# Optimization experiments

Hardware: AMD Instinct MI355X
Metric: run time of the kernel (lower is better)

## Reference

```python
import jax, jax.numpy as jnp
import numpy as np

B, N, C = 4, 8192, 128
NPOINT, NSAMPLE = 2048, 32
RADIUS = 0.1
EPS = 1e-5  # BatchNorm eps (eval mode with running stats)


def setup_inputs() -> dict:
    key = jax.random.key(0)
    k1, k2, k3 = jax.random.split(key, 3)
    return {
        "points_coor": jax.random.uniform(k1, (B, 3, N), dtype=jnp.float32),
        "points_fea": jax.random.normal(k2, (B, C, N), dtype=jnp.float32),
        "W": jax.random.normal(k3, (2 * C, C + 3), dtype=jnp.float32) * 0.05,
        "b": jnp.zeros((2 * C,), jnp.float32),
        "gamma": jnp.ones((2 * C,), jnp.float32),
        "beta": jnp.zeros((2 * C,), jnp.float32),
        "bn_mean": jnp.zeros((2 * C,), jnp.float32),
        "bn_var": jnp.ones((2 * C,), jnp.float32),
    }


def _fps_single(xyz):
    """Farthest point sampling for one cloud. xyz: (N,3) -> (NPOINT,) int32.
    Deterministic start at index 0 (torch version starts at a random index)."""
    n = xyz.shape[0]

    def body(carry, _):
        dist, farthest = carry
        centroid = xyz[farthest]                      # (3,)
        d = jnp.sum((xyz - centroid) ** 2, axis=-1)   # (N,)
        dist = jnp.minimum(dist, d)
        nxt = jnp.argmax(dist).astype(jnp.int32)
        return (dist, nxt), farthest

    init = (jnp.full((n,), 1e10, xyz.dtype), jnp.int32(0))
    (_, _), idx = jax.lax.scan(body, init, None, length=NPOINT)
    return idx


def _gather(points, idx):
    # points: (B,N,D), idx: (B,S,K) -> (B,S,K,D)
    return jax.vmap(lambda p, i: p[i])(points, idx)


def reference(points_coor, points_fea, W, b, gamma, beta, bn_mean, bn_var):
    coor = points_coor.transpose(0, 2, 1)  # (B,N,3)
    fea = points_fea.transpose(0, 2, 1)    # (B,N,C)

    # S: farthest point sampling
    fps_idx = jax.vmap(_fps_single)(coor)                              # (B,S)
    new_coor = jnp.take_along_axis(coor, fps_idx[:, :, None], axis=1)  # (B,S,3)

    # G: hybrid knn/ball query -- k nearest, out-of-radius replaced by nearest
    sq = (jnp.sum(new_coor ** 2, -1)[:, :, None]
          + jnp.sum(coor ** 2, -1)[:, None, :]
          - 2.0 * jnp.einsum('bsd,bnd->bsn', new_coor, coor))           # (B,S,N)
    neg_d, idx = jax.lax.top_k(-sq, NSAMPLE)                            # k smallest
    d = -neg_d
    group_idx = jnp.where(d > RADIUS ** 2, idx[:, :, 0:1], idx)         # (B,S,K)

    g_coor = (_gather(coor, group_idx) - new_coor[:, :, None, :]) / RADIUS  # (B,S,K,3)
    g_fea = _gather(fea, group_idx)                                         # (B,S,K,C)
    g = jnp.concatenate([g_fea, g_coor], axis=-1)                           # (B,S,K,C+3)

    # P: shared 1x1 conv + BN(eval) + ReLU, then max-pool over neighbors
    h = jnp.einsum('bskc,dc->bskd', g, W) + b
    h = gamma * (h - bn_mean) * jax.lax.rsqrt(bn_var + EPS) + beta
    h = jax.nn.relu(h)
    new_fea = jnp.max(h, axis=2)  # (B,S,2C)

    return new_coor.transpose(0, 2, 1), new_fea.transpose(0, 2, 1)
```

## Files before the change

kernel.cpp:

```cpp
#include <hip/hip_runtime.h>
#include <stdint.h>


typedef unsigned short u16;
typedef unsigned long long u64;
typedef __bf16 bf16x8 __attribute__((ext_vector_type(8)));
typedef float f32x4 __attribute__((ext_vector_type(4)));
typedef float f32x2 __attribute__((ext_vector_type(2)));

#define NB 4
#define NPTS 8192
#define CH 128
#define SPTS 2048
#define KN 32
#define CINP 160

__device__ __forceinline__ u16 f2b(float f) {
    unsigned x = __float_as_uint(f);
    unsigned r = (x + 0x7fffu + ((x >> 16) & 1u)) >> 16;
    return (u16)r;
}
__device__ __forceinline__ u64 umin64(u64 a, u64 b) { return a < b ? a : b; }
__device__ __forceinline__ int mort3(int v) {
    return (v & 1) | ((v & 2) << 2) | ((v & 4) << 4);
}

template <int CTRL>
__device__ __forceinline__ u64 dpp_max64(u64 k) {
    unsigned lo = (unsigned)k, hi = (unsigned)(k >> 32);
    unsigned mlo = (unsigned)__builtin_amdgcn_update_dpp((int)lo, (int)lo, CTRL, 0xF, 0xF, false);
    unsigned mhi = (unsigned)__builtin_amdgcn_update_dpp((int)hi, (int)hi, CTRL, 0xF, 0xF, false);
    u64 m = ((u64)mhi << 32) | mlo;
    return m > k ? m : k;
}
template <int CTRL>
__device__ __forceinline__ unsigned dpp_maxu(unsigned v) {
    unsigned mv = (unsigned)__builtin_amdgcn_update_dpp((int)v, (int)v, CTRL, 0xF, 0xF, false);
    return mv > v ? mv : v;
}

__global__ __launch_bounds__(256) void ksort(const float* __restrict__ coor,
                                             float* __restrict__ sxg,
                                             float* __restrict__ syg,
                                             float* __restrict__ szg,
                                             int* __restrict__ sog) {
    __shared__ int hist[512], base[512];
    int b = blockIdx.x, tid = threadIdx.x;
    const float* cb = coor + b * 3 * NPTS;
    hist[tid] = 0;
    hist[tid + 256] = 0;
    __syncthreads();
    int bins[32];
#pragma unroll 4
    for (int i = 0; i < 32; ++i) {
        int n = tid * 32 + i;
        float x = cb[n], y = cb[NPTS + n], z = cb[2 * NPTS + n];
        int bx = min(7, (int)(x * 8.0f));
        int by = min(7, (int)(y * 8.0f));
        int bz = min(7, (int)(z * 8.0f));
        int bin = mort3(bx) | (mort3(by) << 1) | (mort3(bz) << 2);
        bins[i] = bin;
        atomicAdd(&hist[bin], 1);
    }
    __syncthreads();
    if (tid == 0) {
        int acc = 0;
        for (int k2 = 0; k2 < 512; ++k2) { base[k2] = acc; acc += hist[k2]; hist[k2] = 0; }
    }
    __syncthreads();
#pragma unroll 4
    for (int i = 0; i < 32; ++i) {
        int n = tid * 32 + i;
        int bin = bins[i];
        int pos = base[bin] + atomicAdd(&hist[bin], 1);
        sxg[b * NPTS + pos] = cb[n];
        syg[b * NPTS + pos] = cb[NPTS + n];
        szg[b * NPTS + pos] = cb[2 * NPTS + n];
        sog[b * NPTS + pos] = n;
    }
}

__global__ __launch_bounds__(1024) void kfps(const float* __restrict__ sxg,
                                             const float* __restrict__ syg,
                                             const float* __restrict__ szg,
                                             const int* __restrict__ sog,
                                             int* __restrict__ fpsIdx,
                                             float* __restrict__ outCoor,
                                             const float* __restrict__ fea,
                                             const float* __restrict__ coor,
                                             const float* __restrict__ W,
                                             u16* __restrict__ feaT,
                                             float* __restrict__ pp,
                                             u16* __restrict__ Wpad) {
    __shared__ float4 sp[NPTS];
    __shared__ unsigned sWin[SPTS];
    __shared__ u64 sAtom[4];
    __shared__ int slot0s;
    int bid = blockIdx.x;
    int tid = threadIdx.x;
    if (bid >= 4) {
        if (bid < 68) {
            u16(*T)[130] = (u16(*)[130])sp;
            int base_t = (bid - 4) * 4;
#pragma unroll 1
            for (int k = 0; k < 4; ++k) {
                int tidx = base_t + k;
                int b = tidx >> 6, nt = tidx & 63;
                int n0 = nt * 128;
#pragma unroll 4
                for (int it = 0; it < 16; ++it) {
                    int idx = it * 1024 + tid;
                    int c = idx >> 7, nl = idx & 127;
                    T[nl][c] = f2b(fea[((size_t)(b * CH + c)) * NPTS + n0 + nl]);
                }
                __syncthreads();
#pragma unroll 4
                for (int it = 0; it < 16; ++it) {
                    int idx = it * 1024 + tid;
                    int nl = idx >> 7, c = idx & 127;
                    feaT[((size_t)(b * NPTS + n0 + nl)) * CH + c] = T[nl][c];
                }
                __syncthreads();
            }
        } else if (bid < 100) {
            int gid = (bid - 68) * 1024 + tid;
            int n = gid & 8191, b = gid >> 13;
            const float* cb = coor + b * 3 * NPTS;
            float x = cb[n], y = cb[NPTS + n], z = cb[2 * NPTS + n];
            pp[gid] = __fadd_rn(__fadd_rn(__fmul_rn(x, x), __fmul_rn(y, y)),
                                __fmul_rn(z, z));
        } else {
            int i = (bid - 100) * 1024 + tid;
            int d = i / CINP, k = i - d * CINP;
            Wpad[i] = (k < 131) ? f2b(W[d * 131 + k]) : (u16)0;
        }
        return;
    }
    int b = bid;
    int lane = tid & 63;
    const float* gx = sxg + b * NPTS;
    const float* gy = syg + b * NPTS;
    const float* gz = szg + b * NPTS;
    const int* go = sog + b * NPTS;
    f32x2 X2[4], Y2[4], Z2[4], D2[4];
    unsigned PK[8];
    int n0 = tid * 8;
    if (tid < 4) sAtom[tid] = 0;
    float lox, hix, loy, hiy, loz, hiz;
#pragma unroll
    for (int j = 0; j < 8; ++j) {
        float x = gx[n0 + j], y = gy[n0 + j], z = gz[n0 + j];
        sp[n0 + j] = make_float4(x, y, z, 0.0f);
        X2[j >> 1][j & 1] = x; Y2[j >> 1][j & 1] = y; Z2[j >> 1][j & 1] = z;
        D2[j >> 1][j & 1] = 1e10f;
        int oi = go[n0 + j];
        PK[j] = ((unsigned)oi << 16) | (unsigned)(n0 + j);
        if (oi == 0) slot0s = n0 + j;
        if (j == 0) {
            lox = hix = x; loy = hiy = y; loz = hiz = z;
        } else {
            lox = fminf(lox, x); hix = fmaxf(hix, x);
            loy = fminf(loy, y); hiy = fmaxf(hiy, y);
            loz = fminf(loz, z); hiz = fmaxf(hiz, z);
        }
    }
    __syncthreads();
    int far = slot0s;
    if (tid == 0) sWin[0] = (unsigned)slot0s;
    float lm = 3.4e38f;
    u64 cachedKey = 1;
    for (int t = 1; t < SPTS; ++t) {
        float4 c = sp[far];
        float fx = c.x, fy = c.y, fz = c.z;
        float ddx = fmaxf(0.0f, fmaxf(lox - fx, fx - hix));
        float ddy = fmaxf(0.0f, fmaxf(loy - fy, fy - hiy));
        float ddz = fmaxf(0.0f, fmaxf(loz - fz, fz - hiz));
        float dmin2 = ddx * ddx + ddy * ddy + ddz * ddz;
        if (__ballot(dmin2 * 0.9995f < lm) != 0ull) {
            {
#pragma clang fp contract(off)
                f32x2 fx2 = {fx, fx}, fy2 = {fy, fy}, fz2 = {fz, fz};
#pragma unroll
                for (int i = 0; i < 4; ++i) {
                    f32x2 dx = X2[i] - fx2;
                    f32x2 dy = Y2[i] - fy2;
                    f32x2 dz = Z2[i] - fz2;
                    f32x2 s = (dx * dx + dy * dy) + dz * dz;
                    D2[i] = __builtin_elementwise_min(D2[i], s);
                }
            }
            f32x2 t01 = __builtin_elementwise_max(D2[0], D2[1]);
            f32x2 t23 = __builtin_elementwise_max(D2[2], D2[3]);
            f32x2 t03 = __builtin_elementwise_max(t01, t23);
            float m = fmaxf(t03[0], t03[1]);
            lm = m;
            unsigned sel = 0xFFFFFFFFu;
#pragma unroll
            for (int j = 0; j < 8; ++j) {
                float dj = D2[j >> 1][j & 1];
                sel = (dj == m) ? (sel < PK[j] ? sel : PK[j]) : sel;
            }
            unsigned mbits = __float_as_uint(m);
            unsigned r = mbits;
            r = dpp_maxu<0xB1>(r);
            r = dpp_maxu<0x4E>(r);
            r = dpp_maxu<0x141>(r);
            r = dpp_maxu<0x140>(r);
            r = dpp_maxu<0x142>(r);
            r = dpp_maxu<0x143>(r);
            unsigned wmaxb = (unsigned)__builtin_amdgcn_readlane((int)r, 63);
            u64 ball = __ballot(mbits == wmaxb);
            unsigned wpk;
            if (__popcll(ball) == 1) {
                int l = __ffsll(ball) - 1;
                wpk = (unsigned)__builtin_amdgcn_readlane((int)sel, l);
            } else {
                u64 kk = (mbits == wmaxb) ? (((u64)wmaxb << 32) | (unsigned)~sel) : 0ull;
                kk = dpp_max64<0xB1>(kk);
                kk = dpp_max64<0x4E>(kk);
                kk = dpp_max64<0x141>(kk);
                kk = dpp_max64<0x140>(kk);
                kk = dpp_max64<0x142>(kk);
                kk = dpp_max64<0x143>(kk);
                unsigned lo = (unsigned)__builtin_amdgcn_readlane((int)(unsigned)kk, 63);
                wpk = ~lo;
            }
            cachedKey = ((u64)wmaxb << 32) | (unsigned)~wpk;
        }
        if (lane == 63) atomicMax(&sAtom[t & 3], cachedKey);
        if (tid == 0) sAtom[(t + 1) & 3] = 0;
        __syncthreads();
        u64 wk = sAtom[t & 3];
        unsigned pk = ~(unsigned)wk;
        far = (int)(pk & 0xFFFFu);
        if (tid == 0) sWin[t] = pk;
    }
    __syncthreads();
    for (int i = tid; i < SPTS; i += 1024) {
        unsigned pk = sWin[i];
        int slot = (int)(pk & 0xFFFFu);
        float4 c = sp[slot];
        fpsIdx[b * SPTS + i] = (int)(pk >> 16);
        float* oc = outCoor + b * 3 * SPTS + i;
        oc[0] = c.x; oc[SPTS] = c.y; oc[2 * SPTS] = c.z;
    }
}

__global__ __launch_bounds__(256) void kgroup(const float* __restrict__ coor,
                                              const float* __restrict__ pp,
                                              const int* __restrict__ fpsIdx,
                                              int* __restrict__ gidxOut) {
    __shared__ u64 buf[4][256];
    __shared__ int cnt[4];
    int tid = threadIdx.x;
    int wv = tid >> 6, lane = tid & 63;
    if (tid < 4) cnt[tid] = 0;
    __syncthreads();
    int row = blockIdx.x * 4 + wv;
    int b = row >> 11, s = row & 2047;
    const float* cb = coor + b * 3 * NPTS;
    int n0 = fpsIdx[b * SPTS + s];
    float cx = cb[n0], cy = cb[NPTS + n0], cz = cb[2 * NPTS + n0];
    float cc = __fadd_rn(__fadd_rn(__fmul_rn(cx, cx), __fmul_rn(cy, cy)),
                         __fmul_rn(cz, cz));
    const float* ppb = pp + b * NPTS;
    u64 mk = ~0ull;
    for (int n = lane; n < NPTS; n += 64) {
        float x = cb[n], y = cb[NPTS + n], z = cb[2 * NPTS + n];
        float dot = __fmaf_rn(cz, z, __fmaf_rn(cy, y, __fmul_rn(cx, x)));
        float sq = __fsub_rn(__fadd_rn(cc, ppb[n]), __fmul_rn(2.0f, dot));
        unsigned ub = __float_as_uint(sq);
        ub ^= (ub >> 31) ? 0xFFFFFFFFu : 0x80000000u;
        u64 key = ((u64)ub << 32) | (unsigned)n;
        mk = umin64(mk, key);
        if (sq <= 0.01f) {
            int p = atomicAdd(&cnt[wv], 1);
            if (p < 256) buf[wv][p] = key;
        }
    }
#pragma unroll
    for (int off = 32; off > 0; off >>= 1) mk = umin64(mk, __shfl_xor(mk, off));
    int C = cnt[wv];
    if (C > 256) C = 256;
    int* go = gidxOut + row * KN;
    if (C <= 32) {
        if (lane < 32) {
            unsigned idx = (lane < C) ? (unsigned)buf[wv][lane] : (unsigned)mk;
            go[lane] = (int)idx;
        }
    } else {
        u64 e[4];
#pragma unroll
        for (int i = 0; i < 4; ++i) {
            int j2 = lane + (i << 6);
            e[i] = (j2 < C) ? buf[wv][j2] : ~0ull;
        }
        int cl = 0;
        unsigned sel = 0;
        for (int it = 0; it < 32; ++it) {
            u64 lb = ~0ull;
            int li = 0;
#pragma unroll
            for (int i = 0; i < 4; ++i) {
                bool f = (((cl >> i) & 1) == 0) && (e[i] < lb);
                lb = f ? e[i] : lb;
                li = f ? i : li;
            }
            u64 wmin = lb;
#pragma unroll
            for (int off = 32; off > 0; off >>= 1) wmin = umin64(wmin, __shfl_xor(wmin, off));
            u64 bal = __ballot(lb == wmin);
            int src = __ffsll((unsigned long long)bal) - 1;
            if (lane == src) cl |= (1 << li);
            if (lane == it) sel = (unsigned)wmin;
        }
        if (lane < 32) go[lane] = (int)sel;
    }
}

__global__ __launch_bounds__(256) void kfeat(const float* __restrict__ coor,
                                             const u16* __restrict__ feaT,
                                             const u16* __restrict__ Wpad,
                                             const float* __restrict__ bias,
                                             const float* __restrict__ gamma,
                                             const float* __restrict__ beta,
                                             const float* __restrict__ bmean,
                                             const float* __restrict__ bvar,
                                             const int* __restrict__ fpsIdx,
                                             const int* __restrict__ gidx,
                                             float* __restrict__ outFea) {
    __shared__ u16 g[KN][168];
    int row = blockIdx.x;
    int b = row >> 11, s = row & 2047;
    int tid = threadIdx.x;
    {
        int k = tid >> 3, j = tid & 7;
        const float* cb = coor + b * 3 * NPTS;
        int nc = fpsIdx[b * SPTS + s];
        int nbr = gidx[row * KN + k];
        const uint4* f4 = (const uint4*)(feaT + (((size_t)b * NPTS + nbr) << 7));
        uint4* gr = (uint4*)&g[k][0];
        gr[j] = f4[j];
        gr[j + 8] = f4[j + 8];
        for (int c = 128 + j; c < CINP; c += 8) {
            u16 v = 0;
            if (c < 131) {
                int dim = c - 128;
                float pv = cb[dim * NPTS + nbr];
                float cv = cb[dim * NPTS + nc];
                v = f2b(__fdiv_rn(__fsub_rn(pv, cv), 0.1f));
            }
            g[k][c] = v;
        }
    }
    __syncthreads();
    int w = tid >> 6, lane = tid & 63;
    int mrow = lane & 15, q = lane >> 4;
    f32x4 acc[4][2] = {};
#pragma unroll
    for (int ks = 0; ks < 5; ++ks) {
        int kb = ks * 32 + q * 8;
        bf16x8 b0 = *(const bf16x8*)&g[mrow][kb];
        bf16x8 b1 = *(const bf16x8*)&g[mrow + 16][kb];
#pragma unroll
        for (int mt = 0; mt < 4; ++mt) {
            bf16x8 a = *(const bf16x8*)&Wpad[(size_t)(w * 64 + mt * 16 + mrow) * CINP + kb];
            acc[mt][0] = __builtin_amdgcn_mfma_f32_16x16x32_bf16(a, b0, acc[mt][0], 0, 0, 0);
            acc[mt][1] = __builtin_amdgcn_mfma_f32_16x16x32_bf16(a, b1, acc[mt][1], 0, 0, 0);
        }
    }
#pragma unroll
    for (int mt = 0; mt < 4; ++mt) {
#pragma unroll
        for (int r = 0; r < 4; ++r) {
            int m = w * 64 + mt * 16 + q * 4 + r;
            float ga = gamma[m], be = beta[m];
            float mu = bmean[m], va = bvar[m], bi = bias[m];
            float rs = 1.0f / sqrtf(va + 1e-5f);
            float h0 = acc[mt][0][r] + bi;
            h0 = fmaxf(ga * (h0 - mu) * rs + be, 0.0f);
            float h1 = acc[mt][1][r] + bi;
            h1 = fmaxf(ga * (h1 - mu) * rs + be, 0.0f);
            float v = fmaxf(h0, h1);
#pragma unroll
            for (int off = 1; off < 16; off <<= 1) v = fmaxf(v, __shfl_xor(v, off));
            if (mrow == 0) outFea[((size_t)(b * 256 + m)) * SPTS + s] = v;
        }
    }
}

extern "C" void kernel_launch(void* const* d_in, const int* in_sizes, int n_in,
                              void* d_out, int out_size, void* d_ws, size_t ws_size,
                              hipStream_t stream) {
    const float* coor = (const float*)d_in[0];
    const float* fea = (const float*)d_in[1];
    const float* W = (const float*)d_in[2];
    const float* bias = (const float*)d_in[3];
    const float* gamma = (const float*)d_in[4];
    const float* beta = (const float*)d_in[5];
    const float* bmean = (const float*)d_in[6];
    const float* bvar = (const float*)d_in[7];
    char* ws = (char*)d_ws;
    int* fpsIdx = (int*)ws;
    int* gidx = (int*)(ws + 32768);
    float* pp = (float*)(ws + 32768 + 1048576);
    u16* feaT = (u16*)(ws + 1212416);
    u16* Wpad = (u16*)(ws + 9601024);
    float* sxg = (float*)(ws + 9682944);
    float* syg = (float*)(ws + 9814016);
    float* szg = (float*)(ws + 9945088);
    int* sog = (int*)(ws + 10076160);
    float* outC = (float*)d_out;
    float* outF = outC + NB * 3 * SPTS;

    ksort<<<NB, 256, 0, stream>>>(coor, sxg, syg, szg, sog);
    kfps<<<140, 1024, 0, stream>>>(sxg, syg, szg, sog, fpsIdx, outC,
                                   fea, coor, W, feaT, pp, Wpad);
    kgroup<<<2048, 256, 0, stream>>>(coor, pp, fpsIdx, gidx);
    kfeat<<<8192, 256, 0, stream>>>(coor, feaT, Wpad, bias, gamma, beta, bmean, bvar,
                                    fpsIdx, gidx, outF);
}
```

Measured before the change: 1.528 ms.

## Fuse FPS, grouping and feature MLP into one persistent kernel with progress counters

```diff
diff --git a/kernel.cpp b/kernel.cpp
--- a/kernel.cpp
+++ b/kernel.cpp
@@ -43,9 +43,11 @@
                                              float* __restrict__ sxg,
                                              float* __restrict__ syg,
                                              float* __restrict__ szg,
-                                             int* __restrict__ sog) {
+                                             int* __restrict__ sog,
+                                             int* __restrict__ ctrs) {
     __shared__ int hist[512], base[512];
     int b = blockIdx.x, tid = threadIdx.x;
+    if (b == 0 && tid < 8) ctrs[tid] = 0;
     const float* cb = coor + b * 3 * NPTS;
     hist[tid] = 0;
     hist[tid + 256] = 0;
@@ -80,59 +82,217 @@
     }
 }
 
-__global__ __launch_bounds__(1024) void kfps(const float* __restrict__ sxg,
-                                             const float* __restrict__ syg,
-                                             const float* __restrict__ szg,
-                                             const int* __restrict__ sog,
-                                             int* __restrict__ fpsIdx,
-                                             float* __restrict__ outCoor,
-                                             const float* __restrict__ fea,
-                                             const float* __restrict__ coor,
-                                             const float* __restrict__ W,
-                                             u16* __restrict__ feaT,
-                                             float* __restrict__ pp,
-                                             u16* __restrict__ Wpad) {
+__global__ __launch_bounds__(1024) void kmega(const float* __restrict__ sxg,
+                                              const float* __restrict__ syg,
+                                              const float* __restrict__ szg,
+                                              const int* __restrict__ sog,
+                                              int* __restrict__ fpsIdx,
+                                              float* __restrict__ outCoor,
+                                              const float* __restrict__ fea,
+                                              const float* __restrict__ coor,
+                                              const float* __restrict__ W,
+                                              u16* __restrict__ feaT,
+                                              float* __restrict__ pp,
+                                              u16* __restrict__ Wpad,
+                                              const float* __restrict__ bias,
+                                              const float* __restrict__ gamma,
+                                              const float* __restrict__ beta,
+                                              const float* __restrict__ bmean,
+                                              const float* __restrict__ bvar,
+                                              float* __restrict__ outFea,
+                                              int* __restrict__ ctrs) {
     __shared__ float4 sp[NPTS];
     __shared__ unsigned sWin[SPTS];
     __shared__ u64 sAtom[4];
     __shared__ int slot0s;
+    __shared__ int sBase;
     int bid = blockIdx.x;
     int tid = threadIdx.x;
+
     if (bid >= 4) {
-        if (bid < 68) {
-            u16(*T)[130] = (u16(*)[130])sp;
-            int base_t = (bid - 4) * 4;
-#pragma unroll 1
-            for (int k = 0; k < 4; ++k) {
-                int tidx = base_t + k;
-                int b = tidx >> 6, nt = tidx & 63;
+        int wid = bid - 4;
+        for (int c = wid; c < 328; c += 252) {
+            if (c < 256) {
+                u16(*T)[130] = (u16(*)[130])sp;
+                int b = c >> 6, nt = c & 63;
                 int n0 = nt * 128;
 #pragma unroll 4
                 for (int it = 0; it < 16; ++it) {
                     int idx = it * 1024 + tid;
-                    int c = idx >> 7, nl = idx & 127;
-                    T[nl][c] = f2b(fea[((size_t)(b * CH + c)) * NPTS + n0 + nl]);
+                    int cc = idx >> 7, nl = idx & 127;
+                    T[nl][cc] = f2b(fea[((size_t)(b * CH + cc)) * NPTS + n0 + nl]);
                 }
                 __syncthreads();
 #pragma unroll 4
                 for (int it = 0; it < 16; ++it) {
                     int idx = it * 1024 + tid;
-                    int nl = idx >> 7, c = idx & 127;
-                    feaT[((size_t)(b * NPTS + n0 + nl)) * CH + c] = T[nl][c];
-                }
+                    int nl = idx >> 7, cc = idx & 127;
+                    feaT[((size_t)(b * NPTS + n0 + nl)) * CH + cc] = T[nl][cc];
+                }
+            } else if (c < 288) {
+                int gid = (c - 256) * 1024 + tid;
+                int n = gid & 8191, b = gid >> 13;
+                const float* cb = coor + b * 3 * NPTS;
+                float x = cb[n], y = cb[NPTS + n], z = cb[2 * NPTS + n];
+                pp[gid] = __fadd_rn(__fadd_rn(__fmul_rn(x, x), __fmul_rn(y, y)),
+                                    __fmul_rn(z, z));
+            } else {
+                int i = (c - 288) * 1024 + tid;
+                int d = i / CINP, k = i - d * CINP;
+                Wpad[i] = (k < 131) ? f2b(W[d * 131 + k]) : (u16)0;
+            }
+            __syncthreads();
+        }
+        __threadfence();
+        __syncthreads();
+        if (tid == 0) {
+            atomicAdd(&ctrs[4], 1);
+            while (__hip_atomic_load(&ctrs[4], __ATOMIC_ACQUIRE,
+                                     __HIP_MEMORY_SCOPE_AGENT) < 252)
+                __builtin_amdgcn_s_sleep(8);
+        }
+        __syncthreads();
+        u64(*buf)[256] = (u64(*)[256])sp;
+        int* cnt = (int*)((char*)sp + 32768);
+        unsigned(*gsel)[KN] = (unsigned(*)[KN])((char*)sp + 32896);
+        u16(*g4)[KN][168] = (u16(*)[KN][168])((char*)sp + 34944);
+        int wv = tid >> 6, lane = tid & 63;
+        for (;;) {
+            if (tid == 0) sBase = atomicAdd(&ctrs[5], 16);
+            __syncthreads();
+            int lbase = sBase;
+            if (lbase >= NB * SPTS) break;
+            if (tid == 0) {
+                int need = ((lbase + 15) >> 2) + 1;
+                for (int bb = 0; bb < 4; ++bb)
+                    while (__hip_atomic_load(&ctrs[bb], __ATOMIC_ACQUIRE,
+                                             __HIP_MEMORY_SCOPE_AGENT) < need)
+                        __builtin_amdgcn_s_sleep(8);
+            }
+            __syncthreads();
+            {
+                int r = lbase + wv, bb = r & 3, s = r >> 2;
+                if (lane == 0) cnt[wv] = 0;
+                const float* cb = coor + bb * 3 * NPTS;
+                int n0 = fpsIdx[bb * SPTS + s];
+                float cx = cb[n0], cy = cb[NPTS + n0], cz = cb[2 * NPTS + n0];
+                float cc = __fadd_rn(__fadd_rn(__fmul_rn(cx, cx), __fmul_rn(cy, cy)),
+                                     __fmul_rn(cz, cz));
+                const float* ppb = pp + bb * NPTS;
+                u64 mk = ~0ull;
+                for (int n = lane; n < NPTS; n += 64) {
+                    float x = cb[n], y = cb[NPTS + n], z = cb[2 * NPTS + n];
+                    float dot = __fmaf_rn(cz, z, __fmaf_rn(cy, y, __fmul_rn(cx, x)));
+                    float sq = __fsub_rn(__fadd_rn(cc, ppb[n]), __fmul_rn(2.0f, dot));
+                    unsigned ub = __float_as_uint(sq);
+                    ub ^= (ub >> 31) ? 0xFFFFFFFFu : 0x80000000u;
+                    u64 key = ((u64)ub << 32) | (unsigned)n;
+                    mk = umin64(mk, key);
+                    if (sq <= 0.01f) {
+                        int p = atomicAdd(&cnt[wv], 1);
+                        if (p < 256) buf[wv][p] = key;
+                    }
+                }
+#pragma unroll
+                for (int off = 32; off > 0; off >>= 1) mk = umin64(mk, __shfl_xor(mk, off));
+                int C = cnt[wv];
+                if (C > 256) C = 256;
+                if (C <= 32) {
+                    if (lane < 32) {
+                        unsigned idx = (lane < C) ? (unsigned)buf[wv][lane] : (unsigned)mk;
+                        gsel[wv][lane] = idx;
+                    }
+                } else {
+                    u64 e[4];
+#pragma unroll
+                    for (int i = 0; i < 4; ++i) {
+                        int j2 = lane + (i << 6);
+                        e[i] = (j2 < C) ? buf[wv][j2] : ~0ull;
+                    }
+                    int cl = 0;
+                    unsigned sel = 0;
+                    for (int it = 0; it < 32; ++it) {
+                        u64 lb = ~0ull;
+                        int li = 0;
+#pragma unroll
+                        for (int i = 0; i < 4; ++i) {
+                            bool f = (((cl >> i) & 1) == 0) && (e[i] < lb);
+                            lb = f ? e[i] : lb;
+                            li = f ? i : li;
+                        }
+                        u64 wmin = lb;
+#pragma unroll
+                        for (int off = 32; off > 0; off >>= 1)
+                            wmin = umin64(wmin, __shfl_xor(wmin, off));
+                        u64 bal = __ballot(lb == wmin);
+                        int src = __ffsll((unsigned long long)bal) - 1;
+                        if (lane == src) cl |= (1 << li);
+                        if (lane == it) sel = (unsigned)wmin;
+                    }
+                    if (lane < 32) gsel[wv][lane] = sel;
+                }
+            }
+            __syncthreads();
+            for (int it4 = 0; it4 < 4; ++it4) {
                 __syncthreads();
-            }
-        } else if (bid < 100) {
-            int gid = (bid - 68) * 1024 + tid;
-            int n = gid & 8191, b = gid >> 13;
-            const float* cb = coor + b * 3 * NPTS;
-            float x = cb[n], y = cb[NPTS + n], z = cb[2 * NPTS + n];
-            pp[gid] = __fadd_rn(__fadd_rn(__fmul_rn(x, x), __fmul_rn(y, y)),
-                                __fmul_rn(z, z));
-        } else {
-            int i = (bid - 100) * 1024 + tid;
-            int d = i / CINP, k = i - d * CINP;
-            Wpad[i] = (k < 131) ? f2b(W[d * 131 + k]) : (u16)0;
+                int g256 = tid >> 8, t256 = tid & 255;
+                int rloc = it4 * 4 + g256;
+                int r2 = lbase + rloc, b2 = r2 & 3, s2 = r2 >> 2;
+                {
+                    int k = t256 >> 3, j = t256 & 7;
+                    const float* cb2 = coor + b2 * 3 * NPTS;
+                    int nc = fpsIdx[b2 * SPTS + s2];
+                    int nbr = (int)gsel[rloc][k];
+                    const uint4* f4p = (const uint4*)(feaT + (((size_t)b2 * NPTS + nbr) << 7));
+                    uint4* gr = (uint4*)&g4[g256][k][0];
+                    gr[j] = f4p[j];
+                    gr[j + 8] = f4p[j + 8];
+                    for (int cch = 128 + j; cch < CINP; cch += 8) {
+                        u16 v = 0;
+                        if (cch < 131) {
+                            int dim = cch - 128;
+                            float pv = cb2[dim * NPTS + nbr];
+                            float cv = cb2[dim * NPTS + nc];
+                            v = f2b(__fdiv_rn(__fsub_rn(pv, cv), 0.1f));
+                        }
+                        g4[g256][k][cch] = v;
+                    }
+                }
+                __syncthreads();
+                int w = t256 >> 6, lane2 = t256 & 63;
+                int mrow = lane2 & 15, q = lane2 >> 4;
+                f32x4 acc[4][2] = {};
+#pragma unroll
+                for (int ks = 0; ks < 5; ++ks) {
+                    int kb = ks * 32 + q * 8;
+                    bf16x8 b0 = *(const bf16x8*)&g4[g256][mrow][kb];
+                    bf16x8 b1 = *(const bf16x8*)&g4[g256][mrow + 16][kb];
+#pragma unroll
+                    for (int mt = 0; mt < 4; ++mt) {
+                        bf16x8 a = *(const bf16x8*)&Wpad[(size_t)(w * 64 + mt * 16 + mrow) * CINP + kb];
+                        acc[mt][0] = __builtin_amdgcn_mfma_f32_16x16x32_bf16(a, b0, acc[mt][0], 0, 0, 0);
+                        acc[mt][1] = __builtin_amdgcn_mfma_f32_16x16x32_bf16(a, b1, acc[mt][1], 0, 0, 0);
+                    }
+                }
+#pragma unroll
+                for (int mt = 0; mt < 4; ++mt) {
+#pragma unroll
+                    for (int r = 0; r < 4; ++r) {
+                        int m = w * 64 + mt * 16 + q * 4 + r;
+                        float ga = gamma[m], be = beta[m];
+                        float mu = bmean[m], va = bvar[m], bi = bias[m];
+                        float rs = 1.0f / sqrtf(va + 1e-5f);
+                        float h0 = acc[mt][0][r] + bi;
+                        h0 = fmaxf(ga * (h0 - mu) * rs + be, 0.0f);
+                        float h1 = acc[mt][1][r] + bi;
+                        h1 = fmaxf(ga * (h1 - mu) * rs + be, 0.0f);
+                        float v = fmaxf(h0, h1);
+#pragma unroll
+                        for (int off = 1; off < 16; off <<= 1) v = fmaxf(v, __shfl_xor(v, off));
+                        if (mrow == 0) outFea[((size_t)(b2 * 256 + m)) * SPTS + s2] = v;
+                    }
+                }
+            }
         }
         return;
     }
@@ -234,158 +394,31 @@
         unsigned pk = ~(unsigned)wk;
         far = (int)(pk & 0xFFFFu);
         if (tid == 0) sWin[t] = pk;
+        if ((t & 63) == 0 && tid < 64) {
+            int i = t - 64 + tid;
+            unsigned pk2 = sWin[i];
+            int slot = (int)(pk2 & 0xFFFFu);
+            float4 c4 = sp[slot];
+            fpsIdx[b * SPTS + i] = (int)(pk2 >> 16);
+            float* oc = outCoor + b * 3 * SPTS + i;
+            oc[0] = c4.x; oc[SPTS] = c4.y; oc[2 * SPTS] = c4.z;
+            __threadfence();
+            if (tid == 0)
+                __hip_atomic_store(&ctrs[b], t, __ATOMIC_RELEASE, __HIP_MEMORY_SCOPE_AGENT);
+        }
     }
     __syncthreads();
-    for (int i = tid; i < SPTS; i += 1024) {
-        unsigned pk = sWin[i];
-        int slot = (int)(pk & 0xFFFFu);
-        float4 c = sp[slot];
-        fpsIdx[b * SPTS + i] = (int)(pk >> 16);
+    if (tid < 64) {
+        int i = 1984 + tid;
+        unsigned pk2 = sWin[i];
+        int slot = (int)(pk2 & 0xFFFFu);
+        float4 c4 = sp[slot];
+        fpsIdx[b * SPTS + i] = (int)(pk2 >> 16);
         float* oc = outCoor + b * 3 * SPTS + i;
-        oc[0] = c.x; oc[SPTS] = c.y; oc[2 * SPTS] = c.z;
-    }
-}
-
-__global__ __launch_bounds__(256) void kgroup(const float* __restrict__ coor,
-                                              const float* __restrict__ pp,
-                                              const int* __restrict__ fpsIdx,
-                                              int* __restrict__ gidxOut) {
-    __shared__ u64 buf[4][256];
-    __shared__ int cnt[4];
-    int tid = threadIdx.x;
-    int wv = tid >> 6, lane = tid & 63;
-    if (tid < 4) cnt[tid] = 0;
-    __syncthreads();
-    int row = blockIdx.x * 4 + wv;
-    int b = row >> 11, s = row & 2047;
-    const float* cb = coor + b * 3 * NPTS;
-    int n0 = fpsIdx[b * SPTS + s];
-    float cx = cb[n0], cy = cb[NPTS + n0], cz = cb[2 * NPTS + n0];
-    float cc = __fadd_rn(__fadd_rn(__fmul_rn(cx, cx), __fmul_rn(cy, cy)),
-                         __fmul_rn(cz, cz));
-    const float* ppb = pp + b * NPTS;
-    u64 mk = ~0ull;
-    for (int n = lane; n < NPTS; n += 64) {
-        float x = cb[n], y = cb[NPTS + n], z = cb[2 * NPTS + n];
-        float dot = __fmaf_rn(cz, z, __fmaf_rn(cy, y, __fmul_rn(cx, x)));
-        float sq = __fsub_rn(__fadd_rn(cc, ppb[n]), __fmul_rn(2.0f, dot));
-        unsigned ub = __float_as_uint(sq);
-        ub ^= (ub >> 31) ? 0xFFFFFFFFu : 0x80000000u;
-        u64 key = ((u64)ub << 32) | (unsigned)n;
-        mk = umin64(mk, key);
-        if (sq <= 0.01f) {
-            int p = atomicAdd(&cnt[wv], 1);
-            if (p < 256) buf[wv][p] = key;
-        }
-    }
-#pragma unroll
-    for (int off = 32; off > 0; off >>= 1) mk = umin64(mk, __shfl_xor(mk, off));
-    int C = cnt[wv];
-    if (C > 256) C = 256;
-    int* go = gidxOut + row * KN;
-    if (C <= 32) {
-        if (lane < 32) {
-            unsigned idx = (lane < C) ? (unsigned)buf[wv][lane] : (unsigned)mk;
-            go[lane] = (int)idx;
-        }
-    } else {
-        u64 e[4];
-#pragma unroll
-        for (int i = 0; i < 4; ++i) {
-            int j2 = lane + (i << 6);
-            e[i] = (j2 < C) ? buf[wv][j2] : ~0ull;
-        }
-        int cl = 0;
-        unsigned sel = 0;
-        for (int it = 0; it < 32; ++it) {
-            u64 lb = ~0ull;
-            int li = 0;
-#pragma unroll
-            for (int i = 0; i < 4; ++i) {
-                bool f = (((cl >> i) & 1) == 0) && (e[i] < lb);
-                lb = f ? e[i] : lb;
-                li = f ? i : li;
-            }
-            u64 wmin = lb;
-#pragma unroll
-            for (int off = 32; off > 0; off >>= 1) wmin = umin64(wmin, __shfl_xor(wmin, off));
-            u64 bal = __ballot(lb == wmin);
-            int src = __ffsll((unsigned long long)bal) - 1;
-            if (lane == src) cl |= (1 << li);
-            if (lane == it) sel = (unsigned)wmin;
-        }
-        if (lane < 32) go[lane] = (int)sel;
-    }
-}
-
-__global__ __launch_bounds__(256) void kfeat(const float* __restrict__ coor,
-                                             const u16* __restrict__ feaT,
-                                             const u16* __restrict__ Wpad,
-                                             const float* __restrict__ bias,
-                                             const float* __restrict__ gamma,
-                                             const float* __restrict__ beta,
-                                             const float* __restrict__ bmean,
-                                             const float* __restrict__ bvar,
-                                             const int* __restrict__ fpsIdx,
-                                             const int* __restrict__ gidx,
-                                             float* __restrict__ outFea) {
-    __shared__ u16 g[KN][168];
-    int row = blockIdx.x;
-    int b = row >> 11, s = row & 2047;
-    int tid = threadIdx.x;
-    {
-        int k = tid >> 3, j = tid & 7;
-        const float* cb = coor + b * 3 * NPTS;
-        int nc = fpsIdx[b * SPTS + s];
-        int nbr = gidx[row * KN + k];
-        const uint4* f4 = (const uint4*)(feaT + (((size_t)b * NPTS + nbr) << 7));
-        uint4* gr = (uint4*)&g[k][0];
-        gr[j] = f4[j];
-        gr[j + 8] = f4[j + 8];
-        for (int c = 128 + j; c < CINP; c += 8) {
-            u16 v = 0;
-            if (c < 131) {
-                int dim = c - 128;
-                float pv = cb[dim * NPTS + nbr];
-                float cv = cb[dim * NPTS + nc];
-                v = f2b(__fdiv_rn(__fsub_rn(pv, cv), 0.1f));
-            }
-            g[k][c] = v;
-        }
-    }
-    __syncthreads();
-    int w = tid >> 6, lane = tid & 63;
-    int mrow = lane & 15, q = lane >> 4;
-    f32x4 acc[4][2] = {};
-#pragma unroll
-    for (int ks = 0; ks < 5; ++ks) {
-        int kb = ks * 32 + q * 8;
-        bf16x8 b0 = *(const bf16x8*)&g[mrow][kb];
-        bf16x8 b1 = *(const bf16x8*)&g[mrow + 16][kb];
-#pragma unroll
-        for (int mt = 0; mt < 4; ++mt) {
-            bf16x8 a = *(const bf16x8*)&Wpad[(size_t)(w * 64 + mt * 16 + mrow) * CINP + kb];
-            acc[mt][0] = __builtin_amdgcn_mfma_f32_16x16x32_bf16(a, b0, acc[mt][0], 0, 0, 0);
-            acc[mt][1] = __builtin_amdgcn_mfma_f32_16x16x32_bf16(a, b1, acc[mt][1], 0, 0, 0);
-        }
-    }
-#pragma unroll
-    for (int mt = 0; mt < 4; ++mt) {
-#pragma unroll
-        for (int r = 0; r < 4; ++r) {
-            int m = w * 64 + mt * 16 + q * 4 + r;
-            float ga = gamma[m], be = beta[m];
-            float mu = bmean[m], va = bvar[m], bi = bias[m];
-            float rs = 1.0f / sqrtf(va + 1e-5f);
-            float h0 = acc[mt][0][r] + bi;
-            h0 = fmaxf(ga * (h0 - mu) * rs + be, 0.0f);
-            float h1 = acc[mt][1][r] + bi;
-            h1 = fmaxf(ga * (h1 - mu) * rs + be, 0.0f);
-            float v = fmaxf(h0, h1);
-#pragma unroll
-            for (int off = 1; off < 16; off <<= 1) v = fmaxf(v, __shfl_xor(v, off));
-            if (mrow == 0) outFea[((size_t)(b * 256 + m)) * SPTS + s] = v;
-        }
+        oc[0] = c4.x; oc[SPTS] = c4.y; oc[2 * SPTS] = c4.z;
+        __threadfence();
+        if (tid == 0)
+            __hip_atomic_store(&ctrs[b], 2048, __ATOMIC_RELEASE, __HIP_MEMORY_SCOPE_AGENT);
     }
 }
 
@@ -402,21 +435,19 @@
     const float* bvar = (const float*)d_in[7];
     char* ws = (char*)d_ws;
     int* fpsIdx = (int*)ws;
-    int* gidx = (int*)(ws + 32768);
-    float* pp = (float*)(ws + 32768 + 1048576);
-    u16* feaT = (u16*)(ws + 1212416);
-    u16* Wpad = (u16*)(ws + 9601024);
-    float* sxg = (float*)(ws + 9682944);
-    float* syg = (float*)(ws + 9814016);
-    float* szg = (float*)(ws + 9945088);
-    int* sog = (int*)(ws + 10076160);
+    int* ctrs = (int*)(ws + 32768);
+    float* pp = (float*)(ws + 65536);
+    u16* feaT = (u16*)(ws + 1048576);
+    u16* Wpad = (u16*)(ws + 9437184);
+    float* sxg = (float*)(ws + 9519104);
+    float* syg = (float*)(ws + 9650176);
+    float* szg = (float*)(ws + 9781248);
+    int* sog = (int*)(ws + 9912320);
     float* outC = (float*)d_out;
     float* outF = outC + NB * 3 * SPTS;
 
-    ksort<<<NB, 256, 0, stream>>>(coor, sxg, syg, szg, sog);
-    kfps<<<140, 1024, 0, stream>>>(sxg, syg, szg, sog, fpsIdx, outC,
-                                   fea, coor, W, feaT, pp, Wpad);
-    kgroup<<<2048, 256, 0, stream>>>(coor, pp, fpsIdx, gidx);
-    kfeat<<<8192, 256, 0, stream>>>(coor, feaT, Wpad, bias, gamma, beta, bmean, bvar,
-                                    fpsIdx, gidx, outF);
-}
+    ksort<<<NB, 256, 0, stream>>>(coor, sxg, syg, szg, sog, ctrs);
+    kmega<<<256, 1024, 0, stream>>>(sxg, syg, szg, sog, fpsIdx, outC,
+                                    fea, coor, W, feaT, pp, Wpad,
+                                    bias, gamma, beta, bmean, bvar, outF, ctrs);
+}
```

New measurement: 1.727 ms. 13.0% more time.

## Use Morton-binned sorted points to prune kgroup neighbor search to nearby cells

Applied to the files above, without the earlier changes.

```diff
diff --git a/kernel.cpp b/kernel.cpp
--- a/kernel.cpp
+++ b/kernel.cpp
@@ -14,6 +14,7 @@
 #define SPTS 2048
 #define KN 32
 #define CINP 160
+#define GCAP 1280
 
 __device__ __forceinline__ u16 f2b(float f) {
     unsigned x = __float_as_uint(f);
@@ -43,7 +44,9 @@
                                              float* __restrict__ sxg,
                                              float* __restrict__ syg,
                                              float* __restrict__ szg,
-                                             int* __restrict__ sog) {
+                                             int* __restrict__ sog,
+                                             float* __restrict__ spp,
+                                             int* __restrict__ gbase) {
     __shared__ int hist[512], base[512];
     int b = blockIdx.x, tid = threadIdx.x;
     const float* cb = coor + b * 3 * NPTS;
@@ -68,15 +71,21 @@
         for (int k2 = 0; k2 < 512; ++k2) { base[k2] = acc; acc += hist[k2]; hist[k2] = 0; }
     }
     __syncthreads();
+    gbase[b * 513 + tid] = base[tid];
+    gbase[b * 513 + 256 + tid] = base[256 + tid];
+    if (tid == 0) gbase[b * 513 + 512] = NPTS;
 #pragma unroll 4
     for (int i = 0; i < 32; ++i) {
         int n = tid * 32 + i;
         int bin = bins[i];
         int pos = base[bin] + atomicAdd(&hist[bin], 1);
-        sxg[b * NPTS + pos] = cb[n];
-        syg[b * NPTS + pos] = cb[NPTS + n];
-        szg[b * NPTS + pos] = cb[2 * NPTS + n];
+        float x = cb[n], y = cb[NPTS + n], z = cb[2 * NPTS + n];
+        sxg[b * NPTS + pos] = x;
+        syg[b * NPTS + pos] = y;
+        szg[b * NPTS + pos] = z;
         sog[b * NPTS + pos] = n;
+        spp[b * NPTS + pos] = __fadd_rn(__fadd_rn(__fmul_rn(x, x), __fmul_rn(y, y)),
+                                        __fmul_rn(z, z));
     }
 }
 
@@ -87,10 +96,8 @@
                                              int* __restrict__ fpsIdx,
                                              float* __restrict__ outCoor,
                                              const float* __restrict__ fea,
-                                             const float* __restrict__ coor,
                                              const float* __restrict__ W,
                                              u16* __restrict__ feaT,
-                                             float* __restrict__ pp,
                                              u16* __restrict__ Wpad) {
     __shared__ float4 sp[NPTS];
     __shared__ unsigned sWin[SPTS];
@@ -122,15 +129,8 @@
                 }
                 __syncthreads();
             }
-        } else if (bid < 100) {
-            int gid = (bid - 68) * 1024 + tid;
-            int n = gid & 8191, b = gid >> 13;
-            const float* cb = coor + b * 3 * NPTS;
-            float x = cb[n], y = cb[NPTS + n], z = cb[2 * NPTS + n];
-            pp[gid] = __fadd_rn(__fadd_rn(__fmul_rn(x, x), __fmul_rn(y, y)),
-                                __fmul_rn(z, z));
         } else {
-            int i = (bid - 100) * 1024 + tid;
+            int i = (bid - 68) * 1024 + tid;
             int d = i / CINP, k = i - d * CINP;
             Wpad[i] = (k < 131) ? f2b(W[d * 131 + k]) : (u16)0;
         }
@@ -247,10 +247,16 @@
 }
 
 __global__ __launch_bounds__(256) void kgroup(const float* __restrict__ coor,
-                                              const float* __restrict__ pp,
+                                              const float* __restrict__ sxg,
+                                              const float* __restrict__ syg,
+                                              const float* __restrict__ szg,
+                                              const int* __restrict__ sog,
+                                              const float* __restrict__ spp,
+                                              const int* __restrict__ gbase,
                                               const int* __restrict__ fpsIdx,
                                               int* __restrict__ gidxOut) {
     __shared__ u64 buf[4][256];
+    __shared__ int posA[4][GCAP];
     __shared__ int cnt[4];
     int tid = threadIdx.x;
     int wv = tid >> 6, lane = tid & 63;
@@ -263,19 +269,76 @@
     float cx = cb[n0], cy = cb[NPTS + n0], cz = cb[2 * NPTS + n0];
     float cc = __fadd_rn(__fadd_rn(__fmul_rn(cx, cx), __fmul_rn(cy, cy)),
                          __fmul_rn(cz, cz));
-    const float* ppb = pp + b * NPTS;
+    int bxlo = max(0, (int)floorf((cx - 0.1001f) * 8.0f));
+    int bxhi = min(7, (int)floorf((cx + 0.1001f) * 8.0f));
+    int bylo = max(0, (int)floorf((cy - 0.1001f) * 8.0f));
+    int byhi = min(7, (int)floorf((cy + 0.1001f) * 8.0f));
+    int bzlo = max(0, (int)floorf((cz - 0.1001f) * 8.0f));
+    int bzhi = min(7, (int)floorf((cz + 0.1001f) * 8.0f));
+    int nx = bxhi - bxlo + 1, ny = byhi - bylo + 1, nz = bzhi - bzlo + 1;
+    int nbins = nx * ny * nz;
+    const int* gb = gbase + b * 513;
+    int lo = 0, len = 0;
+    if (lane < nbins) {
+        int lx = lane % nx;
+        int rest = lane / nx;
+        int ly = rest % ny;
+        int lz = rest / ny;
+        int bin = mort3(bxlo + lx) | (mort3(bylo + ly) << 1) | (mort3(bzlo + lz) << 2);
+        lo = gb[bin];
+        len = gb[bin + 1] - lo;
+    }
+    int v = len;
+#pragma unroll
+    for (int off = 1; off < 64; off <<= 1) {
+        int u = __shfl_up(v, off);
+        if (lane >= off) v += u;
+    }
+    int T = __shfl(v, 63);
+    int pfe = v - len;
+    bool fast = (T <= GCAP);
+    if (fast) {
+        for (int i = 0; i < len; ++i) posA[wv][pfe + i] = lo + i;
+    }
+    __syncthreads();
+    const float* bx_ = sxg + b * NPTS;
+    const float* by_ = syg + b * NPTS;
+    const float* bz_ = szg + b * NPTS;
+    const int* bo_ = sog + b * NPTS;
+    const float* bp_ = spp + b * NPTS;
     u64 mk = ~0ull;
-    for (int n = lane; n < NPTS; n += 64) {
-        float x = cb[n], y = cb[NPTS + n], z = cb[2 * NPTS + n];
-        float dot = __fmaf_rn(cz, z, __fmaf_rn(cy, y, __fmul_rn(cx, x)));
-        float sq = __fsub_rn(__fadd_rn(cc, ppb[n]), __fmul_rn(2.0f, dot));
-        unsigned ub = __float_as_uint(sq);
-        ub ^= (ub >> 31) ? 0xFFFFFFFFu : 0x80000000u;
-        u64 key = ((u64)ub << 32) | (unsigned)n;
-        mk = umin64(mk, key);
-        if (sq <= 0.01f) {
-            int p = atomicAdd(&cnt[wv], 1);
-            if (p < 256) buf[wv][p] = key;
+    if (fast) {
+        for (int j = lane; j < T; j += 64) {
+            int p = posA[wv][j];
+            float x = bx_[p], y = by_[p], z = bz_[p];
+            float ppv = bp_[p];
+            int oi = bo_[p];
+            float dot = __fmaf_rn(cz, z, __fmaf_rn(cy, y, __fmul_rn(cx, x)));
+            float sq = __fsub_rn(__fadd_rn(cc, ppv), __fmul_rn(2.0f, dot));
+            unsigned ub = __float_as_uint(sq);
+            ub ^= (ub >> 31) ? 0xFFFFFFFFu : 0x80000000u;
+            u64 key = ((u64)ub << 32) | (unsigned)oi;
+            mk = umin64(mk, key);
+            if (sq <= 0.01f) {
+                int p2 = atomicAdd(&cnt[wv], 1);
+                if (p2 < 256) buf[wv][p2] = key;
+            }
+        }
+    } else {
+        for (int n = lane; n < NPTS; n += 64) {
+            float x = cb[n], y = cb[NPTS + n], z = cb[2 * NPTS + n];
+            float ppv = __fadd_rn(__fadd_rn(__fmul_rn(x, x), __fmul_rn(y, y)),
+                                  __fmul_rn(z, z));
+            float dot = __fmaf_rn(cz, z, __fmaf_rn(cy, y, __fmul_rn(cx, x)));
+            float sq = __fsub_rn(__fadd_rn(cc, ppv), __fmul_rn(2.0f, dot));
+            unsigned ub = __float_as_uint(sq);
+            ub ^= (ub >> 31) ? 0xFFFFFFFFu : 0x80000000u;
+            u64 key = ((u64)ub << 32) | (unsigned)n;
+            mk = umin64(mk, key);
+            if (sq <= 0.01f) {
+                int p2 = atomicAdd(&cnt[wv], 1);
+                if (p2 < 256) buf[wv][p2] = key;
+            }
         }
     }
 #pragma unroll
@@ -402,21 +465,23 @@
     const float* bvar = (const float*)d_in[7];
     char* ws = (char*)d_ws;
     int* fpsIdx = (int*)ws;
-    int* gidx = (int*)(ws + 32768);
-    float* pp = (float*)(ws + 32768 + 1048576);
-    u16* feaT = (u16*)(ws + 1212416);
-    u16* Wpad = (u16*)(ws + 9601024);
-    float* sxg = (float*)(ws + 9682944);
-    float* syg = (float*)(ws + 9814016);
-    float* szg = (float*)(ws + 9945088);
-    int* sog = (int*)(ws + 10076160);
+    float* spp = (float*)(ws + 32768);
+    int* gbase = (int*)(ws + 163840);
+    int* gidx = (int*)(ws + 180224);
+    u16* feaT = (u16*)(ws + 1228800);
+    u16* Wpad = (u16*)(ws + 9617408);
+    float* sxg = (float*)(ws + 9699328);
+    float* syg = (float*)(ws + 9830400);
+    float* szg = (float*)(ws + 9961472);
+    int* sog = (int*)(ws + 10092544);
     float* outC = (float*)d_out;
     float* outF = outC + NB * 3 * SPTS;
 
-    ksort<<<NB, 256, 0, stream>>>(coor, sxg, syg, szg, sog);
-    kfps<<<140, 1024, 0, stream>>>(sxg, syg, szg, sog, fpsIdx, outC,
-                                   fea, coor, W, feaT, pp, Wpad);
-    kgroup<<<2048, 256, 0, stream>>>(coor, pp, fpsIdx, gidx);
+    ksort<<<NB, 256, 0, stream>>>(coor, sxg, syg, szg, sog, spp, gbase);
+    kfps<<<108, 1024, 0, stream>>>(sxg, syg, szg, sog, fpsIdx, outC,
+                                   fea, W, feaT, Wpad);
+    kgroup<<<2048, 256, 0, stream>>>(coor, sxg, syg, szg, sog, spp, gbase,
+                                     fpsIdx, gidx);
     kfeat<<<8192, 256, 0, stream>>>(coor, feaT, Wpad, bias, gamma, beta, bmean, bvar,
                                     fpsIdx, gidx, outF);
 }
```

After: 1.491 ms. 1.03x faster.
